# Performance work log

Measured on AMD Instinct MI355X. Metric: run time of the kernel, lower is better.

Reference implementation:

```python
import jax, jax.numpy as jnp
import numpy as np
from jax.scipy.special import gammaln

DIM = 64
N_FT = 1024
X_RANGE = 0.3
TWO_PI = 2.0 * np.pi


def gaussian_kernel_fun_ft(k, dim, scale_sq):
    # 1D Fourier coefficients of the sliced Gaussian kernel exp(-r^2/(2 sigma^2)):
    # f_hat(k) = pi^{d/2}/Gamma(d/2) * (2 pi sigma^2)^{d/2} * |k|^{d-1} * exp(-2 pi^2 sigma^2 k^2)
    # computed in log-space for stability at large d.
    logk = jnp.log(jnp.maximum(jnp.abs(k), 1e-30))
    log_f = (
        0.5 * dim * jnp.log(jnp.float32(np.pi))
        + 0.5 * dim * jnp.log(TWO_PI * scale_sq)
        - gammaln(jnp.float32(dim / 2.0))
        + (dim - 1) * logk
        - 2.0 * jnp.float32(np.pi**2) * scale_sq * k**2
    )
    return jnp.where(k == 0, jnp.float32(0.0), jnp.exp(log_f))


def setup_inputs() -> dict:
    key = jax.random.key(0)
    k1, k2, k3, k4 = jax.random.split(key, 4)
    N, M, P = 8192, 8192, 16
    return {
        "x": jax.random.normal(k1, (N, DIM), dtype=jnp.float32),
        "y": jax.random.normal(k2, (M, DIM), dtype=jnp.float32),
        "x_weights": jax.random.normal(k3, (N,), dtype=jnp.float32),
        "xis": jax.random.normal(k4, (P, DIM), dtype=jnp.float32),
        "scale": 10,
        "P": P,
    }


def reference(x, y, x_weights, xis, scale, P):
    # rescale all points into the ball of radius x_range (as fastsum_fft does)
    scale_f = jnp.float32(scale)
    max_norm = jnp.maximum(
        jnp.max(jnp.sqrt(jnp.sum(x**2, -1))), jnp.max(jnp.sqrt(jnp.sum(y**2, -1)))
    )
    sf = X_RANGE / max_norm
    xs = x * sf  # (N, d)
    ys = y * sf  # (M, d)
    s = scale_f * sf

    h = jnp.arange(-N_FT // 2, N_FT // 2, dtype=x.dtype)  # (K,) frequencies
    kft = gaussian_kernel_fun_ft(h, DIM, s**2)  # (K,)

    # get_xis: normalize random directions onto the unit sphere
    xis_n = xis / jnp.sqrt(jnp.sum(xis**2, -1, keepdims=True))  # (P, d)

    def body(acc, xi):
        xp = TWO_PI * (xs @ xi)  # (N,) projected source nodes, times 2*pi
        yp = TWO_PI * (ys @ xi)  # (M,)
        # adjoint NDFT: a_k = sum_i w_i e^{2 pi i k x_i}, split into real trig sums
        a_re = kft * (x_weights @ jnp.cos(xp[:, None] * h))  # (K,)
        a_im = kft * (x_weights @ jnp.sin(xp[:, None] * h))  # (K,)
        # forward NDFT at targets, real part of sum_k a_k kft_k e^{-2 pi i k y_j}
        out_p = jnp.cos(yp[:, None] * h) @ a_re + jnp.sin(yp[:, None] * h) @ a_im
        return acc + out_p, None

    acc, _ = jax.lax.scan(body, jnp.zeros(y.shape[0], x.dtype), xis_n)
    return acc / jnp.float32(xis_n.shape[0])  # average over the P slices
```

## Files before the change

### kernel.cpp

```cpp
#include <hip/hip_runtime.h>
#include <math.h>

#define DIM   64
#define PMAX  16
#define KMAXA 64
#define KREG  16
#define NBLKA 64
#define CH    16

#define WS_BLOCKMAX 0
#define WS_SF       64
#define WS_KMAX     65
#define WS_ARE      128
#define WS_AIM      (WS_ARE + PMAX*KMAXA)
#define WS_RPX      (WS_AIM + PMAX*KMAXA)

__global__ void __launch_bounds__(256) k_prep(
    const float* __restrict__ x, const float* __restrict__ y,
    const float* __restrict__ xis, float* __restrict__ wsF,
    int N, int M, int P)
{
    __shared__ __align__(16) float sxi[PMAX * DIM];
    __shared__ float sinv[PMAX];
    __shared__ float sred[4];
    const int tid = threadIdx.x;
    const int gtid = blockIdx.x * blockDim.x + tid;
    const int gsz = gridDim.x * blockDim.x;

    for (int idx = tid * 4; idx < P * DIM; idx += blockDim.x * 4)
        *(float4*)(sxi + idx) = *(const float4*)(xis + idx);
    __syncthreads();
    if (tid < P) {
        float ss = 0.f;
        for (int d = 0; d < DIM; ++d) { float v = sxi[tid * DIM + d]; ss += v * v; }
        sinv[tid] = 1.0f / sqrtf(ss);
    }
    __syncthreads();

    if (gtid < 2 * PMAX * KMAXA) wsF[WS_ARE + gtid] = 0.f;

    float mx = 0.f;
    const int rows = N + M;
    for (int r = gtid; r < rows; r += gsz) {
        const float4* rowp = (const float4*)((r < N) ? (x + (size_t)r * DIM)
                                                     : (y + (size_t)(r - N) * DIM));
        float ss = 0.f;
        float acc[PMAX];
#pragma unroll
        for (int p = 0; p < PMAX; ++p) acc[p] = 0.f;
#pragma unroll
        for (int d4 = 0; d4 < DIM / 4; ++d4) {
            float4 v = rowp[d4];
            ss += v.x * v.x + v.y * v.y + v.z * v.z + v.w * v.w;
#pragma unroll
            for (int p = 0; p < PMAX; ++p) {
                float4 w = *(const float4*)(sxi + p * DIM + d4 * 4);
                acc[p] = fmaf(v.x, w.x, fmaf(v.y, w.y, fmaf(v.z, w.z, fmaf(v.w, w.w, acc[p]))));
            }
        }
        mx = fmaxf(mx, ss);
        float* dst = wsF + WS_RPX + ((r < N) ? (size_t)0 : (size_t)P * N);
        int   rr   = (r < N) ? r : r - N;
        int   L    = (r < N) ? N : M;
#pragma unroll
        for (int p = 0; p < PMAX; ++p)
            dst[(size_t)p * L + rr] = acc[p] * sinv[p];
    }
    for (int off = 32; off; off >>= 1) mx = fmaxf(mx, __shfl_down(mx, off));
    if ((tid & 63) == 0) sred[tid >> 6] = mx;
    __syncthreads();
    if (tid == 0) {
        float m = fmaxf(fmaxf(sred[0], sred[1]), fmaxf(sred[2], sred[3]));
        wsF[WS_BLOCKMAX + blockIdx.x] = m;
    }
}

__global__ void __launch_bounds__(256) k_adj(
    const float* __restrict__ xw, const int* __restrict__ scale_raw,
    float* __restrict__ wsF, int N, int P)
{
    __shared__ float skft[KMAXA];
    __shared__ float sacc[2 * KMAXA];
    __shared__ int   s_kmax;
    __shared__ float s_sf;
    const int tid = threadIdx.x;
    const int bid = blockIdx.x;

    float m = (tid < NBLKA) ? wsF[WS_BLOCKMAX + tid] : 0.f;
    for (int off = 32; off; off >>= 1) m = fmaxf(m, __shfl_down(m, off));
    if (tid == 0) { s_sf = 0.3f / sqrtf(m); s_kmax = 0; }
    __syncthreads();
    const float sf = s_sf;

    int iv = *scale_raw;
    float scale_f = (iv > -1000000 && iv < 1000000) ? (float)iv : __int_as_float(iv);
    float s2 = (scale_f * sf) * (scale_f * sf);
    if (tid < KMAXA) {
        int k = tid + 1;
        float kf = (float)k;
        const float C0 = 36.63135635f - 78.09222355f;
        float lf = C0 + 32.0f * logf(6.2831853071795864f * s2) + 63.0f * logf(kf)
                 - 19.739208802178716f * s2 * kf * kf;
        float kft = expf(lf);
        skft[tid] = kft;
        if (kft > 0.f) atomicMax(&s_kmax, k);
    }
    for (int i = tid; i < 2 * KMAXA; i += blockDim.x) sacc[i] = 0.f;
    __syncthreads();
    const int kmax = s_kmax;

    const int pp = bid % P;
    const int c  = bid / P;
    const int NCH = gridDim.x / P;
    const float* rp = wsF + WS_RPX + (size_t)pp * N;
    const int chunk = (N + NCH - 1) / NCH;
    const int i0 = c * chunk, i1 = min(N, i0 + chunk);

    for (int kb = 0; kb < kmax; kb += KREG) {
        float accRe[KREG], accIm[KREG];
#pragma unroll
        for (int t = 0; t < KREG; ++t) { accRe[t] = 0.f; accIm[t] = 0.f; }
        for (int i = i0 + tid; i < i1; i += blockDim.x) {
            float w = xw[i];
            float proj = sf * rp[i];
#pragma unroll
            for (int t = 0; t < KREG; ++t) {
                int k = kb + 1 + t;
                if (k <= kmax) {
                    float r = proj * (float)k;
                    r -= rintf(r);
                    accRe[t] = fmaf(w, __builtin_amdgcn_cosf(r), accRe[t]);
                    accIm[t] = fmaf(w, __builtin_amdgcn_sinf(r), accIm[t]);
                }
            }
        }
#pragma unroll
        for (int t = 0; t < KREG; ++t) {
            int k = kb + 1 + t;
            if (k <= kmax) {
                for (int off = 32; off; off >>= 1) {
                    accRe[t] += __shfl_down(accRe[t], off);
                    accIm[t] += __shfl_down(accIm[t], off);
                }
                if ((tid & 63) == 0) {
                    atomicAdd(&sacc[2 * (k - 1)],     accRe[t]);
                    atomicAdd(&sacc[2 * (k - 1) + 1], accIm[t]);
                }
            }
        }
    }
    __syncthreads();
    if (tid < kmax) {
        float kf = skft[tid];
        atomicAdd(wsF + WS_ARE + pp * KMAXA + tid, sacc[2 * tid] * kf);
        atomicAdd(wsF + WS_AIM + pp * KMAXA + tid, sacc[2 * tid + 1] * kf);
    }
    if (bid == 0 && tid == 0) {
        wsF[WS_SF] = sf;
        ((int*)wsF)[WS_KMAX] = kmax;
    }
}

__global__ void __launch_bounds__(256) k_fwd(
    float* __restrict__ out, const float* __restrict__ wsF, int N, int M, int P)
{
    __shared__ float sa[2 * PMAX * KMAXA];
    const int tid = threadIdx.x;
    const float sf = wsF[WS_SF];
    const int kmax = ((const int*)wsF)[WS_KMAX];
    for (int i = tid; i < P * kmax; i += blockDim.x) {
        int pp = i / kmax, kk = i % kmax;
        sa[2 * i]     = wsF[WS_ARE + pp * KMAXA + kk];
        sa[2 * i + 1] = wsF[WS_AIM + pp * KMAXA + kk];
    }
    __syncthreads();
    const float* rpy = wsF + WS_RPX + (size_t)P * N;
    const float invP2 = 2.0f / (float)P;
    for (int j = blockIdx.x * blockDim.x + tid; j < M; j += gridDim.x * blockDim.x) {
        float acc = 0.f;
        for (int pp = 0; pp < P; ++pp) {
            float proj = sf * rpy[(size_t)pp * M + j];
            const float* ap = sa + 2 * pp * kmax;
            for (int kk = 0; kk < kmax; ++kk) {
                float r = proj * (float)(kk + 1);
                r -= rintf(r);
                acc = fmaf(__builtin_amdgcn_cosf(r), ap[2 * kk], acc);
                acc = fmaf(__builtin_amdgcn_sinf(r), ap[2 * kk + 1], acc);
            }
        }
        out[j] = acc * invP2;
    }
}

extern "C" void kernel_launch(void* const* d_in, const int* in_sizes, int n_in,
                              void* d_out, int out_size, void* d_ws, size_t ws_size,
                              hipStream_t stream) {
    const float* x   = (const float*)d_in[0];
    const float* y   = (const float*)d_in[1];
    const float* xw  = (const float*)d_in[2];
    const float* xis = (const float*)d_in[3];
    const int* scale_raw = (const int*)d_in[4];
    float* wsF = (float*)d_ws;
    int N = in_sizes[0] / DIM;
    int M = in_sizes[1] / DIM;
    int P = in_sizes[3] / DIM;

    k_prep<<<NBLKA, 256, 0, stream>>>(x, y, xis, wsF, N, M, P);
    k_adj<<<P * CH, 256, 0, stream>>>(xw, scale_raw, wsF, N, P);
    k_fwd<<<(M + 255) / 256, 256, 0, stream>>>((float*)d_out, wsF, N, M, P);
}
```

Measured before the change: 98.02 us.

## Fuse prep, adjoint and forward stages into one persistent kernel with grid barriers

Merges the three stage kernels into a single persistent kernel of 256 blocks that uses atomic-counter grid barriers between stages, plus a small init kernel that zeroes counters, coefficients and the output. The forward stage is split eight ways across slice groups and accumulated with atomics, so more threads run the trig sums for the 8192 targets. The prep stage now runs on 256 blocks instead of 64. The aim is to remove inter-kernel launch gaps and raise parallelism. In exchange it relies on every block being co-resident for the spin barriers, and it adds atomic contention on the output.

```diff
diff --git a/kernel.cpp b/kernel.cpp
--- a/kernel.cpp
+++ b/kernel.cpp
@@ -5,27 +5,57 @@
 #define PMAX  16
 #define KMAXA 64
 #define KREG  16
-#define NBLKA 64
-#define CH    16
-
-#define WS_BLOCKMAX 0
-#define WS_SF       64
-#define WS_KMAX     65
-#define WS_ARE      128
+#define NBLK  256
+#define NTHR  256
+
+#define WS_BAR0     0
+#define WS_BAR1     1
+#define WS_BLOCKMAX 16
+#define WS_ARE      (16 + NBLK)
 #define WS_AIM      (WS_ARE + PMAX*KMAXA)
 #define WS_RPX      (WS_AIM + PMAX*KMAXA)
 
-__global__ void __launch_bounds__(256) k_prep(
+__global__ void __launch_bounds__(256) k_init(float* __restrict__ wsF,
+                                              float* __restrict__ out, int M) {
+    int gtid = blockIdx.x * blockDim.x + threadIdx.x;
+    int gsz = gridDim.x * blockDim.x;
+    if (gtid == 0) { ((int*)wsF)[WS_BAR0] = 0; ((int*)wsF)[WS_BAR1] = 0; }
+    for (int i = gtid; i < 2 * PMAX * KMAXA; i += gsz) wsF[WS_ARE + i] = 0.f;
+    for (int i = gtid; i < M; i += gsz) out[i] = 0.f;
+}
+
+__device__ inline void gbar(int* cnt, int nblk) {
+    __syncthreads();
+    if (threadIdx.x == 0) {
+        __threadfence();
+        __hip_atomic_fetch_add(cnt, 1, __ATOMIC_ACQ_REL, __HIP_MEMORY_SCOPE_AGENT);
+        while (__hip_atomic_load(cnt, __ATOMIC_ACQUIRE, __HIP_MEMORY_SCOPE_AGENT) < nblk)
+            __builtin_amdgcn_s_sleep(2);
+        __threadfence();
+    }
+    __syncthreads();
+}
+
+__global__ void __launch_bounds__(NTHR) k_main(
     const float* __restrict__ x, const float* __restrict__ y,
-    const float* __restrict__ xis, float* __restrict__ wsF,
-    int N, int M, int P)
+    const float* __restrict__ xw, const float* __restrict__ xis,
+    const int* __restrict__ scale_raw, float* __restrict__ out,
+    float* __restrict__ wsF, int N, int M, int P)
 {
     __shared__ __align__(16) float sxi[PMAX * DIM];
     __shared__ float sinv[PMAX];
-    __shared__ float sred[4];
-    const int tid = threadIdx.x;
-    const int gtid = blockIdx.x * blockDim.x + tid;
-    const int gsz = gridDim.x * blockDim.x;
+    __shared__ float sred[NTHR / 64];
+    __shared__ float skft[KMAXA];
+    __shared__ float sacc[2 * KMAXA];
+    __shared__ float sa[2 * PMAX * KMAXA];
+    __shared__ int   s_kmax;
+    __shared__ float s_sf;
+
+    const int tid  = threadIdx.x;
+    const int bid  = blockIdx.x;
+    const int gsz  = gridDim.x * blockDim.x;
+    const int gtid = bid * blockDim.x + tid;
+    int* bars = (int*)wsF;
 
     for (int idx = tid * 4; idx < P * DIM; idx += blockDim.x * 4)
         *(float4*)(sxi + idx) = *(const float4*)(xis + idx);
@@ -36,8 +66,6 @@
         sinv[tid] = 1.0f / sqrtf(ss);
     }
     __syncthreads();
-
-    if (gtid < 2 * PMAX * KMAXA) wsF[WS_ARE + gtid] = 0.f;
 
     float mx = 0.f;
     const int rows = N + M;
@@ -70,28 +98,26 @@
     if ((tid & 63) == 0) sred[tid >> 6] = mx;
     __syncthreads();
     if (tid == 0) {
-        float m = fmaxf(fmaxf(sred[0], sred[1]), fmaxf(sred[2], sred[3]));
-        wsF[WS_BLOCKMAX + blockIdx.x] = m;
-    }
-}
-
-__global__ void __launch_bounds__(256) k_adj(
-    const float* __restrict__ xw, const int* __restrict__ scale_raw,
-    float* __restrict__ wsF, int N, int P)
-{
-    __shared__ float skft[KMAXA];
-    __shared__ float sacc[2 * KMAXA];
-    __shared__ int   s_kmax;
-    __shared__ float s_sf;
-    const int tid = threadIdx.x;
-    const int bid = blockIdx.x;
-
-    float m = (tid < NBLKA) ? wsF[WS_BLOCKMAX + tid] : 0.f;
+        float m = sred[0];
+        for (int w = 1; w < NTHR / 64; ++w) m = fmaxf(m, sred[w]);
+        wsF[WS_BLOCKMAX + bid] = m;
+    }
+
+    gbar(bars + WS_BAR0, gridDim.x);
+
+    float m = (tid < NBLK) ? wsF[WS_BLOCKMAX + tid] : 0.f;
+    for (int i = tid + NTHR; i < (int)gridDim.x; i += NTHR) m = fmaxf(m, wsF[WS_BLOCKMAX + i]);
     for (int off = 32; off; off >>= 1) m = fmaxf(m, __shfl_down(m, off));
-    if (tid == 0) { s_sf = 0.3f / sqrtf(m); s_kmax = 0; }
+    if ((tid & 63) == 0) sred[tid >> 6] = m;
+    __syncthreads();
+    if (tid == 0) {
+        float mm = sred[0];
+        for (int w = 1; w < NTHR / 64; ++w) mm = fmaxf(mm, sred[w]);
+        s_sf = 0.3f / sqrtf(mm);
+        s_kmax = 0;
+    }
     __syncthreads();
     const float sf = s_sf;
-
     int iv = *scale_raw;
     float scale_f = (iv > -1000000 && iv < 1000000) ? (float)iv : __int_as_float(iv);
     float s2 = (scale_f * sf) * (scale_f * sf);
@@ -109,65 +135,56 @@
     __syncthreads();
     const int kmax = s_kmax;
 
-    const int pp = bid % P;
-    const int c  = bid / P;
     const int NCH = gridDim.x / P;
-    const float* rp = wsF + WS_RPX + (size_t)pp * N;
-    const int chunk = (N + NCH - 1) / NCH;
-    const int i0 = c * chunk, i1 = min(N, i0 + chunk);
-
-    for (int kb = 0; kb < kmax; kb += KREG) {
-        float accRe[KREG], accIm[KREG];
-#pragma unroll
-        for (int t = 0; t < KREG; ++t) { accRe[t] = 0.f; accIm[t] = 0.f; }
-        for (int i = i0 + tid; i < i1; i += blockDim.x) {
-            float w = xw[i];
-            float proj = sf * rp[i];
+    if (bid < P * NCH) {
+        const int pp = bid % P;
+        const int c  = bid / P;
+        const float* rp = wsF + WS_RPX + (size_t)pp * N;
+        const int chunk = (N + NCH - 1) / NCH;
+        const int i0 = c * chunk, i1 = min(N, i0 + chunk);
+        for (int kb = 0; kb < kmax; kb += KREG) {
+            float accRe[KREG], accIm[KREG];
+#pragma unroll
+            for (int t = 0; t < KREG; ++t) { accRe[t] = 0.f; accIm[t] = 0.f; }
+            for (int i = i0 + tid; i < i1; i += blockDim.x) {
+                float w = xw[i];
+                float proj = sf * rp[i];
+#pragma unroll
+                for (int t = 0; t < KREG; ++t) {
+                    int k = kb + 1 + t;
+                    if (k <= kmax) {
+                        float r = proj * (float)k;
+                        r -= rintf(r);
+                        accRe[t] = fmaf(w, __builtin_amdgcn_cosf(r), accRe[t]);
+                        accIm[t] = fmaf(w, __builtin_amdgcn_sinf(r), accIm[t]);
+                    }
+                }
+            }
 #pragma unroll
             for (int t = 0; t < KREG; ++t) {
                 int k = kb + 1 + t;
                 if (k <= kmax) {
-                    float r = proj * (float)k;
-                    r -= rintf(r);
-                    accRe[t] = fmaf(w, __builtin_amdgcn_cosf(r), accRe[t]);
-                    accIm[t] = fmaf(w, __builtin_amdgcn_sinf(r), accIm[t]);
+                    for (int off = 32; off; off >>= 1) {
+                        accRe[t] += __shfl_down(accRe[t], off);
+                        accIm[t] += __shfl_down(accIm[t], off);
+                    }
+                    if ((tid & 63) == 0) {
+                        atomicAdd(&sacc[2 * (k - 1)],     accRe[t]);
+                        atomicAdd(&sacc[2 * (k - 1) + 1], accIm[t]);
+                    }
                 }
             }
         }
-#pragma unroll
-        for (int t = 0; t < KREG; ++t) {
-            int k = kb + 1 + t;
-            if (k <= kmax) {
-                for (int off = 32; off; off >>= 1) {
-                    accRe[t] += __shfl_down(accRe[t], off);
-                    accIm[t] += __shfl_down(accIm[t], off);
-                }
-                if ((tid & 63) == 0) {
-                    atomicAdd(&sacc[2 * (k - 1)],     accRe[t]);
-                    atomicAdd(&sacc[2 * (k - 1) + 1], accIm[t]);
-                }
-            }
-        }
-    }
-    __syncthreads();
-    if (tid < kmax) {
-        float kf = skft[tid];
-        atomicAdd(wsF + WS_ARE + pp * KMAXA + tid, sacc[2 * tid] * kf);
-        atomicAdd(wsF + WS_AIM + pp * KMAXA + tid, sacc[2 * tid + 1] * kf);
-    }
-    if (bid == 0 && tid == 0) {
-        wsF[WS_SF] = sf;
-        ((int*)wsF)[WS_KMAX] = kmax;
-    }
-}
-
-__global__ void __launch_bounds__(256) k_fwd(
-    float* __restrict__ out, const float* __restrict__ wsF, int N, int M, int P)
-{
-    __shared__ float sa[2 * PMAX * KMAXA];
-    const int tid = threadIdx.x;
-    const float sf = wsF[WS_SF];
-    const int kmax = ((const int*)wsF)[WS_KMAX];
+        __syncthreads();
+        if (tid < kmax) {
+            float kf = skft[tid];
+            atomicAdd(wsF + WS_ARE + pp * KMAXA + tid, sacc[2 * tid] * kf);
+            atomicAdd(wsF + WS_AIM + pp * KMAXA + tid, sacc[2 * tid + 1] * kf);
+        }
+    }
+
+    gbar(bars + WS_BAR1, gridDim.x);
+
     for (int i = tid; i < P * kmax; i += blockDim.x) {
         int pp = i / kmax, kk = i % kmax;
         sa[2 * i]     = wsF[WS_ARE + pp * KMAXA + kk];
@@ -176,9 +193,10 @@
     __syncthreads();
     const float* rpy = wsF + WS_RPX + (size_t)P * N;
     const float invP2 = 2.0f / (float)P;
-    for (int j = blockIdx.x * blockDim.x + tid; j < M; j += gridDim.x * blockDim.x) {
+    for (int t = gtid; t < M * 8; t += gsz) {
+        int j = t >> 3, pg = t & 7;
         float acc = 0.f;
-        for (int pp = 0; pp < P; ++pp) {
+        for (int pp = pg; pp < P; pp += 8) {
             float proj = sf * rpy[(size_t)pp * M + j];
             const float* ap = sa + 2 * pp * kmax;
             for (int kk = 0; kk < kmax; ++kk) {
@@ -188,7 +206,7 @@
                 acc = fmaf(__builtin_amdgcn_sinf(r), ap[2 * kk + 1], acc);
             }
         }
-        out[j] = acc * invP2;
+        atomicAdd(out + j, acc * invP2);
     }
 }
 
@@ -205,7 +223,7 @@
     int M = in_sizes[1] / DIM;
     int P = in_sizes[3] / DIM;
 
-    k_prep<<<NBLKA, 256, 0, stream>>>(x, y, xis, wsF, N, M, P);
-    k_adj<<<P * CH, 256, 0, stream>>>(xw, scale_raw, wsF, N, P);
-    k_fwd<<<(M + 255) / 256, 256, 0, stream>>>((float*)d_out, wsF, N, M, P);
-}
+    k_init<<<40, 256, 0, stream>>>(wsF, (float*)d_out, M);
+    k_main<<<NBLK, NTHR, 0, stream>>>(x, y, xw, xis, scale_raw,
+                                      (float*)d_out, wsF, N, M, P);
+}
```

After: 134.0 us. 1.37x slower.
